# Kernel optimization log

Measured on AMD Instinct MI355X. Metric: run time of the kernel, lower is better.

Reference implementation:

```python
import jax, jax.numpy as jnp
import numpy as np

IN_F = 4096
OUT_F = 4096
RANK = 8
ALPHA = 8
SCALE = ALPHA / RANK


def setup_inputs() -> dict:
    key = jax.random.key(0)
    kx, kw, kb, ka = jax.random.split(key, 4)
    x = jax.random.normal(kx, (4, 4096, IN_F), dtype=jnp.float32)
    # base frozen linear params (torch Linear default init style, any values ok)
    W = jax.random.normal(kw, (OUT_F, IN_F), dtype=jnp.float32) * (1.0 / np.sqrt(IN_F))
    b = jax.random.normal(kb, (OUT_F,), dtype=jnp.float32) * 0.01
    # lora_A: kaiming_uniform_(a=sqrt(5)) -> U(-bound, bound), bound = sqrt(6/((1+5)*in_f)) = 1/sqrt(in_f)
    bound = 1.0 / np.sqrt(IN_F)
    lora_A = jax.random.uniform(ka, (RANK, IN_F), dtype=jnp.float32, minval=-bound, maxval=bound)
    # lora_B initialized to zeros per module; use small random values so the LoRA path is exercised
    lora_B = jax.random.normal(jax.random.fold_in(key, 7), (OUT_F, RANK), dtype=jnp.float32) * 0.02
    return {"x": x, "W": W, "b": b, "lora_A": lora_A, "lora_B": lora_B}


def reference(x, W, b, lora_A, lora_B):
    # base: x @ W.T + b  [B,S,out_f]
    base = jnp.einsum("bsi,oi->bso", x, W) + b
    # low-rank path: (x @ A.T) @ B.T * scale
    xa = jnp.einsum("bsi,ri->bsr", x, lora_A)  # [B,S,r]
    lora = jnp.einsum("bsr,or->bso", xa, lora_B)
    return base + lora * SCALE
```

## Files before the change

kernel.cpp:

```cpp
#include <hip/hip_runtime.h>
#include <cstdint>

#define K_IN   4096
#define N_OUT  4096
#define M_ROWS 16384
#define RANK   8
#define LSCALE 1.0f
#define NTILES 128

typedef __attribute__((ext_vector_type(8))) short  short8;
typedef __attribute__((ext_vector_type(4))) float  floatx4;

__device__ __forceinline__ unsigned short f2bf(float f) {
  uint32_t u = __float_as_uint(f);
  u += 0x7FFFu + ((u >> 16) & 1u);
  return (unsigned short)(u >> 16);
}

__global__ __launch_bounds__(256) void fold_w_kernel(
    const float* __restrict__ W, const float* __restrict__ lA,
    const float* __restrict__ lB, unsigned short* __restrict__ Weff) {
  int idx = blockIdx.x * 256 + threadIdx.x;
  int o = idx >> 10;
  int k = (idx & 1023) << 2;
  float4 w = *reinterpret_cast<const float4*>(W + (size_t)o * K_IN + k);
#pragma unroll
  for (int r = 0; r < RANK; ++r) {
    float s = LSCALE * lB[o * RANK + r];
    float4 a = *reinterpret_cast<const float4*>(lA + r * K_IN + k);
    w.x += s * a.x; w.y += s * a.y; w.z += s * a.z; w.w += s * a.w;
  }
  ushort4 p;
  p.x = f2bf(w.x); p.y = f2bf(w.y); p.z = f2bf(w.z); p.w = f2bf(w.w);
  *reinterpret_cast<ushort4*>(Weff + (size_t)o * K_IN + k) = p;
}

__global__ __launch_bounds__(256) void cvt_x_kernel(
    const float* __restrict__ x, unsigned short* __restrict__ xb) {
  size_t i = ((size_t)blockIdx.x * 256 + threadIdx.x) * 8;
  float4 a = *reinterpret_cast<const float4*>(x + i);
  float4 c = *reinterpret_cast<const float4*>(x + i + 4);
  uint4 v;
  v.x = (uint32_t)f2bf(a.x) | ((uint32_t)f2bf(a.y) << 16);
  v.y = (uint32_t)f2bf(a.z) | ((uint32_t)f2bf(a.w) << 16);
  v.z = (uint32_t)f2bf(c.x) | ((uint32_t)f2bf(c.y) << 16);
  v.w = (uint32_t)f2bf(c.z) | ((uint32_t)f2bf(c.w) << 16);
  *reinterpret_cast<uint4*>(xb + i) = v;
}

__device__ __forceinline__ void gload_lds16(const void* g, void* l) {
  __builtin_amdgcn_global_load_lds(
      (const __attribute__((address_space(1))) void*)g,
      (__attribute__((address_space(3))) void*)l, 16, 0, 0);
}

__global__ __launch_bounds__(512, 2) void gemm_kernel(
    const unsigned short* __restrict__ Xb, const unsigned short* __restrict__ Wb,
    const float* __restrict__ bias, float* __restrict__ out) {
  __shared__ alignas(16) char lds[4 * 32768];

  const int tid  = threadIdx.x;
  const int wave = tid >> 6, lane = tid & 63;
  const int wr = wave >> 2, wc = wave & 3;
  const int l15 = lane & 15, sq = lane >> 4;

  int bx  = blockIdx.x;
  int sbx = (bx & 7) * 128 + (bx >> 3);
  const int mt = sbx >> 4;
  const int nt = sbx & 15;

  const unsigned short *gA0, *gA1, *gB0, *gB1;
  {
    int L0 = (wave * 2 + 0) * 1024 + lane * 16;
    int r0 = ((L0 >> 7) << 1) | (((L0 >> 6) ^ (L0 >> 8)) & 1);
    int s0 = ((L0 >> 4) & 3) ^ (r0 & 3);
    gA0 = Xb + (size_t)(mt * 256 + r0) * K_IN + s0 * 8;
    gB0 = Wb + (size_t)(nt * 256 + r0) * K_IN + s0 * 8;
    int L1 = (wave * 2 + 1) * 1024 + lane * 16;
    int r1 = ((L1 >> 7) << 1) | (((L1 >> 6) ^ (L1 >> 8)) & 1);
    int s1 = ((L1 >> 4) & 3) ^ (r1 & 3);
    gA1 = Xb + (size_t)(mt * 256 + r1) * K_IN + s1 * 8;
    gB1 = Wb + (size_t)(nt * 256 + r1) * K_IN + s1 * 8;
  }
  const int lo0 = (wave * 2 + 0) * 1024;
  const int lo1 = (wave * 2 + 1) * 1024;

#define STAGE(tt) do {                                        \
    char* base_ = lds + ((tt) & 3) * 32768;                   \
    gload_lds16(gA0 + (tt) * 32, base_ + lo0);                \
    gload_lds16(gB0 + (tt) * 32, base_ + 16384 + lo0);        \
    gload_lds16(gA1 + (tt) * 32, base_ + lo1);                \
    gload_lds16(gB1 + (tt) * 32, base_ + 16384 + lo1);        \
  } while (0)

  floatx4 acc[8][4];
#pragma unroll
  for (int i = 0; i < 8; ++i)
#pragma unroll
    for (int j = 0; j < 4; ++j)
      acc[i][j] = (floatx4){0.f, 0.f, 0.f, 0.f};

  STAGE(0); STAGE(1); STAGE(2);

  const int xorv = (l15 & 7) << 4;

  for (int t = 0; t < NTILES; ++t) {
    if (t < NTILES - 2)       asm volatile("s_waitcnt vmcnt(8)" ::: "memory");
    else if (t == NTILES - 2) asm volatile("s_waitcnt vmcnt(4)" ::: "memory");
    else                      asm volatile("s_waitcnt vmcnt(0)" ::: "memory");
    __builtin_amdgcn_s_barrier();
    asm volatile("" ::: "memory");

    const char* Ab = lds + (t & 3) * 32768;
    const char* Bb = Ab + 16384;
    short8 af[8], bf[4];
#pragma unroll
    for (int i = 0; i < 8; ++i) {
      int rA = wr * 128 + i * 16 + l15;
      int LA = ((rA << 6) | (sq << 4)) ^ xorv;
      af[i] = *reinterpret_cast<const short8*>(Ab + LA);
    }
#pragma unroll
    for (int j = 0; j < 4; ++j) {
      int rB = wc * 64 + j * 16 + l15;
      int LB = ((rB << 6) | (sq << 4)) ^ xorv;
      bf[j] = *reinterpret_cast<const short8*>(Bb + LB);
    }
    asm volatile("s_waitcnt lgkmcnt(0)" ::: "memory");
    __builtin_amdgcn_s_barrier();
    asm volatile("" ::: "memory");

    if (t + 3 < NTILES) STAGE(t + 3);

#pragma unroll
    for (int i = 0; i < 8; ++i)
#pragma unroll
      for (int j = 0; j < 4; ++j)
        acc[i][j] = __builtin_amdgcn_mfma_f32_16x16x32_bf16(af[i], bf[j], acc[i][j], 0, 0, 0);
  }
#undef STAGE

  const int row0 = mt * 256 + wr * 128 + sq * 4;
  const int col0 = nt * 256 + wc * 64 + l15;
#pragma unroll
  for (int j = 0; j < 4; ++j) {
    int col = col0 + j * 16;
    float bv = bias[col];
#pragma unroll
    for (int i = 0; i < 8; ++i) {
      int rowb = row0 + i * 16;
#pragma unroll
      for (int rr = 0; rr < 4; ++rr)
        out[(size_t)(rowb + rr) * N_OUT + col] = acc[i][j][rr] + bv;
    }
  }
}

__global__ __launch_bounds__(256) void fallback_kernel(
    const float* __restrict__ x, const float* __restrict__ W,
    const float* __restrict__ bias, const float* __restrict__ lA,
    const float* __restrict__ lB, float* __restrict__ out) {
  __shared__ float Xs[64][17];
  __shared__ float Ws[64][17];
  int tid = threadIdx.x;
  int tx = tid & 15, ty = tid >> 4;
  int bm = blockIdx.y * 64, bn = blockIdx.x * 64;
  float acc[4][4] = {};
  for (int k0 = 0; k0 < K_IN; k0 += 16) {
#pragma unroll
    for (int q = 0; q < 4; ++q) {
      int flat = q * 256 + tid;
      int r = flat >> 4, c = flat & 15;
      Xs[r][c] = x[(size_t)(bm + r) * K_IN + k0 + c];
      float w = W[(size_t)(bn + r) * K_IN + k0 + c];
#pragma unroll
      for (int rr = 0; rr < RANK; ++rr)
        w += LSCALE * lB[(bn + r) * RANK + rr] * lA[rr * K_IN + k0 + c];
      Ws[r][c] = w;
    }
    __syncthreads();
#pragma unroll
    for (int kk = 0; kk < 16; ++kk) {
      float av[4], bv[4];
#pragma unroll
      for (int i = 0; i < 4; ++i) av[i] = Xs[ty * 4 + i][kk];
#pragma unroll
      for (int j = 0; j < 4; ++j) bv[j] = Ws[tx * 4 + j][kk];
#pragma unroll
      for (int i = 0; i < 4; ++i)
#pragma unroll
        for (int j = 0; j < 4; ++j) acc[i][j] += av[i] * bv[j];
    }
    __syncthreads();
  }
#pragma unroll
  for (int i = 0; i < 4; ++i)
#pragma unroll
    for (int j = 0; j < 4; ++j)
      out[(size_t)(bm + ty * 4 + i) * N_OUT + bn + tx * 4 + j] =
          acc[i][j] + bias[bn + tx * 4 + j];
}

extern "C" void kernel_launch(void* const* d_in, const int* in_sizes, int n_in,
                              void* d_out, int out_size, void* d_ws, size_t ws_size,
                              hipStream_t stream) {
  const float* x  = (const float*)d_in[0];
  const float* W  = (const float*)d_in[1];
  const float* b  = (const float*)d_in[2];
  const float* lA = (const float*)d_in[3];
  const float* lB = (const float*)d_in[4];
  float* out = (float*)d_out;

  const size_t weff_bytes = (size_t)N_OUT * K_IN * 2;
  const size_t xb_bytes   = (size_t)M_ROWS * K_IN * 2;

  if (ws_size >= weff_bytes + xb_bytes) {
    unsigned short* Weff = (unsigned short*)d_ws;
    unsigned short* Xb   = (unsigned short*)((char*)d_ws + weff_bytes);
    fold_w_kernel<<<(int)(((size_t)N_OUT * K_IN / 4) / 256), 256, 0, stream>>>(W, lA, lB, Weff);
    cvt_x_kernel<<<(int)(((size_t)M_ROWS * K_IN / 8) / 256), 256, 0, stream>>>(x, Xb);
    gemm_kernel<<<(M_ROWS / 256) * (N_OUT / 256), 512, 0, stream>>>(Xb, Weff, b, out);
  } else {
    dim3 grid(N_OUT / 64, M_ROWS / 64);
    fallback_kernel<<<grid, 256, 0, stream>>>(x, W, b, lA, lB, out);
  }
}
```

Measured before the change: 711.6 us.

## Restructure GEMM main loop into 8-phase double-buffered schedule with MFMA priority

Replaces the four-stage K=32 LDS ring with two 64 KB buffers, each holding a K=64 tile split into two K-halves. Each tile is processed in four phases that interleave LDS fragment loads, the next tile's global-to-LDS loads, and half of the MFMAs, with s_setprio raised around MFMA bursts. The aim is to overlap memory traffic with compute more finely and to cut register pressure by holding only four A fragments at a time. The cost is many more barriers per K step and shallower prefetch depth, and the hand-placed vmcnt waits must be correct for the LDS reuse to be safe.

```diff
diff --git a/kernel.cpp b/kernel.cpp
--- a/kernel.cpp
+++ b/kernel.cpp
@@ -6,7 +6,7 @@
 #define M_ROWS 16384
 #define RANK   8
 #define LSCALE 1.0f
-#define NTILES 128
+#define NT     64
 
 typedef __attribute__((ext_vector_type(8))) short  short8;
 typedef __attribute__((ext_vector_type(4))) float  floatx4;
@@ -57,12 +57,13 @@
 __global__ __launch_bounds__(512, 2) void gemm_kernel(
     const unsigned short* __restrict__ Xb, const unsigned short* __restrict__ Wb,
     const float* __restrict__ bias, float* __restrict__ out) {
-  __shared__ alignas(16) char lds[4 * 32768];
+  __shared__ alignas(16) char lds[2 * 65536];
 
   const int tid  = threadIdx.x;
   const int wave = tid >> 6, lane = tid & 63;
   const int wr = wave >> 2, wc = wave & 3;
   const int l15 = lane & 15, sq = lane >> 4;
+  const int xorv = (l15 & 7) << 4;
 
   int bx  = blockIdx.x;
   int sbx = (bx & 7) * 128 + (bx >> 3);
@@ -71,27 +72,57 @@
 
   const unsigned short *gA0, *gA1, *gB0, *gB1;
   {
-    int L0 = (wave * 2 + 0) * 1024 + lane * 16;
+    int L0 = tid * 16;
     int r0 = ((L0 >> 7) << 1) | (((L0 >> 6) ^ (L0 >> 8)) & 1);
     int s0 = ((L0 >> 4) & 3) ^ (r0 & 3);
     gA0 = Xb + (size_t)(mt * 256 + r0) * K_IN + s0 * 8;
     gB0 = Wb + (size_t)(nt * 256 + r0) * K_IN + s0 * 8;
-    int L1 = (wave * 2 + 1) * 1024 + lane * 16;
+    int L1 = 8192 + tid * 16;
     int r1 = ((L1 >> 7) << 1) | (((L1 >> 6) ^ (L1 >> 8)) & 1);
     int s1 = ((L1 >> 4) & 3) ^ (r1 & 3);
     gA1 = Xb + (size_t)(mt * 256 + r1) * K_IN + s1 * 8;
     gB1 = Wb + (size_t)(nt * 256 + r1) * K_IN + s1 * 8;
   }
-  const int lo0 = (wave * 2 + 0) * 1024;
-  const int lo1 = (wave * 2 + 1) * 1024;
-
-#define STAGE(tt) do {                                        \
-    char* base_ = lds + ((tt) & 3) * 32768;                   \
-    gload_lds16(gA0 + (tt) * 32, base_ + lo0);                \
-    gload_lds16(gB0 + (tt) * 32, base_ + 16384 + lo0);        \
-    gload_lds16(gA1 + (tt) * 32, base_ + lo1);                \
-    gload_lds16(gB1 + (tt) * 32, base_ + 16384 + lo1);        \
+
+#define STAGE_A(TT, KS) do {                                         \
+    char* d_ = lds + ((TT) & 1) * 65536 + (KS) * 16384 + tid * 16;   \
+    gload_lds16(gA0 + (TT) * 64 + (KS) * 32, d_);                    \
+    gload_lds16(gA1 + (TT) * 64 + (KS) * 32, d_ + 8192);             \
   } while (0)
+#define STAGE_B(TT, KS) do {                                         \
+    char* d_ = lds + ((TT) & 1) * 65536 + 32768 + (KS) * 16384 + tid * 16; \
+    gload_lds16(gB0 + (TT) * 64 + (KS) * 32, d_);                    \
+    gload_lds16(gB1 + (TT) * 64 + (KS) * 32, d_ + 8192);             \
+  } while (0)
+#define BAR() do { asm volatile("" ::: "memory");                    \
+    __builtin_amdgcn_s_barrier();                                    \
+    asm volatile("" ::: "memory"); } while (0)
+#define LGKM0() asm volatile("s_waitcnt lgkmcnt(0)" ::: "memory")
+#define LOAD_AF(MH, KS) do {                                         \
+    const char* Ah_ = lds + tb + (KS) * 16384;                       \
+    _Pragma("unroll")                                                \
+    for (int i = 0; i < 4; ++i) {                                    \
+      int rA_ = wr * 128 + ((MH) * 4 + i) * 16 + l15;                \
+      int LA_ = ((rA_ << 6) | (sq << 4)) ^ xorv;                     \
+      af[i] = *reinterpret_cast<const short8*>(Ah_ + LA_);           \
+    } } while (0)
+#define LOAD_BF(KS) do {                                             \
+    const char* Bh_ = lds + tb + 32768 + (KS) * 16384;               \
+    _Pragma("unroll")                                                \
+    for (int j = 0; j < 4; ++j) {                                    \
+      int rB_ = wc * 64 + j * 16 + l15;                              \
+      int LB_ = ((rB_ << 6) | (sq << 4)) ^ xorv;                     \
+      bf[j] = *reinterpret_cast<const short8*>(Bh_ + LB_);           \
+    } } while (0)
+#define DO_MFMA(MH) do {                                             \
+    __builtin_amdgcn_s_setprio(1);                                   \
+    _Pragma("unroll")                                                \
+    for (int i = 0; i < 4; ++i)                                      \
+      _Pragma("unroll")                                              \
+      for (int j = 0; j < 4; ++j)                                    \
+        acc[(MH) * 4 + i][j] = __builtin_amdgcn_mfma_f32_16x16x32_bf16( \
+            af[i], bf[j], acc[(MH) * 4 + i][j], 0, 0, 0);            \
+    __builtin_amdgcn_s_setprio(0); } while (0)
 
   floatx4 acc[8][4];
 #pragma unroll
@@ -100,45 +131,50 @@
     for (int j = 0; j < 4; ++j)
       acc[i][j] = (floatx4){0.f, 0.f, 0.f, 0.f};
 
-  STAGE(0); STAGE(1); STAGE(2);
-
-  const int xorv = (l15 & 7) << 4;
-
-  for (int t = 0; t < NTILES; ++t) {
-    if (t < NTILES - 2)       asm volatile("s_waitcnt vmcnt(8)" ::: "memory");
-    else if (t == NTILES - 2) asm volatile("s_waitcnt vmcnt(4)" ::: "memory");
-    else                      asm volatile("s_waitcnt vmcnt(0)" ::: "memory");
-    __builtin_amdgcn_s_barrier();
-    asm volatile("" ::: "memory");
-
-    const char* Ab = lds + (t & 3) * 32768;
-    const char* Bb = Ab + 16384;
-    short8 af[8], bf[4];
-#pragma unroll
-    for (int i = 0; i < 8; ++i) {
-      int rA = wr * 128 + i * 16 + l15;
-      int LA = ((rA << 6) | (sq << 4)) ^ xorv;
-      af[i] = *reinterpret_cast<const short8*>(Ab + LA);
-    }
-#pragma unroll
-    for (int j = 0; j < 4; ++j) {
-      int rB = wc * 64 + j * 16 + l15;
-      int LB = ((rB << 6) | (sq << 4)) ^ xorv;
-      bf[j] = *reinterpret_cast<const short8*>(Bb + LB);
-    }
-    asm volatile("s_waitcnt lgkmcnt(0)" ::: "memory");
-    __builtin_amdgcn_s_barrier();
-    asm volatile("" ::: "memory");
-
-    if (t + 3 < NTILES) STAGE(t + 3);
-
-#pragma unroll
-    for (int i = 0; i < 8; ++i)
-#pragma unroll
-      for (int j = 0; j < 4; ++j)
-        acc[i][j] = __builtin_amdgcn_mfma_f32_16x16x32_bf16(af[i], bf[j], acc[i][j], 0, 0, 0);
-  }
-#undef STAGE
+  STAGE_A(0, 0); STAGE_B(0, 0); STAGE_A(0, 1); STAGE_B(0, 1);
+  asm volatile("s_waitcnt vmcnt(4)" ::: "memory");
+  BAR();
+
+  short8 af[4], bf[4];
+
+  for (int t = 0; t < NT; ++t) {
+    const int tb = (t & 1) * 65536;
+    const bool more = (t + 1 < NT);
+
+    LOAD_AF(0, 0);
+    LOAD_BF(0);
+    if (more) STAGE_A(t + 1, 0);
+    BAR(); LGKM0();
+    DO_MFMA(0);
+    BAR();
+
+    LOAD_AF(1, 0);
+    if (more) STAGE_B(t + 1, 0);
+    BAR(); LGKM0();
+    DO_MFMA(1);
+    if (more) asm volatile("s_waitcnt vmcnt(4)" ::: "memory");
+    else      asm volatile("s_waitcnt vmcnt(0)" ::: "memory");
+    BAR();
+
+    LOAD_AF(0, 1);
+    LOAD_BF(1);
+    if (more) STAGE_A(t + 1, 1);
+    BAR(); LGKM0();
+    DO_MFMA(0);
+    BAR();
+
+    LOAD_AF(1, 1);
+    if (more) STAGE_B(t + 1, 1);
+    BAR(); LGKM0();
+    DO_MFMA(1);
+    if (more) asm volatile("s_waitcnt vmcnt(4)" ::: "memory");
+    BAR();
+  }
+#undef STAGE_A
+#undef STAGE_B
+#undef LOAD_AF
+#undef LOAD_BF
+#undef DO_MFMA
 
   const int row0 = mt * 256 + wr * 128 + sq * 4;
   const int col0 = nt * 256 + wc * 64 + l15;
```

Result: faster. 638.9 us (-10.2%).

## Restructure GEMM mainloop into quadrant-interleaved 8-wave ping-pong with K=64 tiles

Applied to the files above, without the earlier changes.

Reworks the bf16 GEMM main loop to use 64-wide K tiles double-buffered in LDS, staged in quarter-tile chunks interleaved between four MFMA quadrant phases separated by barriers. Adds s_setprio around MFMA bursts and a new XOR swizzle for 128-byte rows. The aim is finer-grained overlap of global->LDS loads, LDS reads and MFMA issue, plus fewer iterations. It adds more barriers per iteration and relies on careful vmcnt accounting, which risks correctness or stalls.

```diff
diff --git a/kernel.cpp b/kernel.cpp
--- a/kernel.cpp
+++ b/kernel.cpp
@@ -6,7 +6,9 @@
 #define M_ROWS 16384
 #define RANK   8
 #define LSCALE 1.0f
-#define NTILES 128
+#define NT     64
+#define ROWB   8192
+#define AHALF  1048576
 
 typedef __attribute__((ext_vector_type(8))) short  short8;
 typedef __attribute__((ext_vector_type(4))) float  floatx4;
@@ -57,7 +59,7 @@
 __global__ __launch_bounds__(512, 2) void gemm_kernel(
     const unsigned short* __restrict__ Xb, const unsigned short* __restrict__ Wb,
     const float* __restrict__ bias, float* __restrict__ out) {
-  __shared__ alignas(16) char lds[4 * 32768];
+  __shared__ alignas(16) char lds[2 * 65536];
 
   const int tid  = threadIdx.x;
   const int wave = tid >> 6, lane = tid & 63;
@@ -69,29 +71,59 @@
   const int mt = sbx >> 4;
   const int nt = sbx & 15;
 
-  const unsigned short *gA0, *gA1, *gB0, *gB1;
-  {
-    int L0 = (wave * 2 + 0) * 1024 + lane * 16;
-    int r0 = ((L0 >> 7) << 1) | (((L0 >> 6) ^ (L0 >> 8)) & 1);
-    int s0 = ((L0 >> 4) & 3) ^ (r0 & 3);
-    gA0 = Xb + (size_t)(mt * 256 + r0) * K_IN + s0 * 8;
-    gB0 = Wb + (size_t)(nt * 256 + r0) * K_IN + s0 * 8;
-    int L1 = (wave * 2 + 1) * 1024 + lane * 16;
-    int r1 = ((L1 >> 7) << 1) | (((L1 >> 6) ^ (L1 >> 8)) & 1);
-    int s1 = ((L1 >> 4) & 3) ^ (r1 & 3);
-    gA1 = Xb + (size_t)(mt * 256 + r1) * K_IN + s1 * 8;
-    gB1 = Wb + (size_t)(nt * 256 + r1) * K_IN + s1 * 8;
-  }
-  const int lo0 = (wave * 2 + 0) * 1024;
-  const int lo1 = (wave * 2 + 1) * 1024;
-
-#define STAGE(tt) do {                                        \
-    char* base_ = lds + ((tt) & 3) * 32768;                   \
-    gload_lds16(gA0 + (tt) * 32, base_ + lo0);                \
-    gload_lds16(gB0 + (tt) * 32, base_ + 16384 + lo0);        \
-    gload_lds16(gA1 + (tt) * 32, base_ + lo1);                \
-    gload_lds16(gB1 + (tt) * 32, base_ + 16384 + lo1);        \
+  const int rstg = tid >> 3;
+  const int cbst = ((tid & 7) << 4) ^ (tid & 32);
+  const char* aBase = (const char*)Xb + (size_t)(mt * 256 + rstg) * ROWB + cbst;
+  const char* bBase = (const char*)Wb + (size_t)(nt * 256 + rstg) * ROWB + cbst;
+
+#define STAGE(H) do {                                                     \
+    int th_ = (H) >> 2, hh_ = (H) & 3;                                    \
+    const char* src_ = ((hh_ < 2) ? aBase + (size_t)hh_ * AHALF           \
+                                  : bBase + (size_t)(hh_ - 2) * AHALF)    \
+                       + th_ * 128;                                       \
+    char* dst_ = lds + (th_ & 1) * 65536 + hh_ * 16384 + tid * 16;        \
+    gload_lds16(src_, dst_);                                              \
+    gload_lds16(src_ + (size_t)64 * ROWB, dst_ + 8192);                   \
   } while (0)
+#define BAR() do { asm volatile("" ::: "memory");                         \
+    __builtin_amdgcn_s_barrier();                                         \
+    asm volatile("" ::: "memory"); } while (0)
+#define LDSWZ(ROW, COLB) ((((ROW) << 7) | (COLB)) ^ (((ROW) & 4) << 3))
+#define LOAD_A(DST, MQ) do {                                              \
+    const char* Ab_ = lds + tb + wr * 16384;                              \
+    _Pragma("unroll")                                                     \
+    for (int ks = 0; ks < 2; ++ks)                                        \
+      _Pragma("unroll")                                                   \
+      for (int fi = 0; fi < 4; ++fi) {                                    \
+        int row_ = (MQ) * 64 + fi * 16 + l15;                             \
+        int cb_  = ks * 64 + sq * 16;                                     \
+        DST[ks * 4 + fi] =                                                \
+            *reinterpret_cast<const short8*>(Ab_ + LDSWZ(row_, cb_));     \
+      } } while (0)
+#define LOAD_B(DST, NQ) do {                                              \
+    const char* Bb_ = lds + tb + (2 + (wc >> 1)) * 16384;                 \
+    _Pragma("unroll")                                                     \
+    for (int ks = 0; ks < 2; ++ks)                                        \
+      _Pragma("unroll")                                                   \
+      for (int fj = 0; fj < 2; ++fj) {                                    \
+        int row_ = (wc & 1) * 64 + (NQ) * 32 + fj * 16 + l15;             \
+        int cb_  = ks * 64 + sq * 16;                                     \
+        DST[ks * 2 + fj] =                                                \
+            *reinterpret_cast<const short8*>(Bb_ + LDSWZ(row_, cb_));     \
+      } } while (0)
+#define MFMA_Q(MQ, NQ, AF, BF) do {                                       \
+    __builtin_amdgcn_s_setprio(1);                                        \
+    _Pragma("unroll")                                                     \
+    for (int ks = 0; ks < 2; ++ks)                                        \
+      _Pragma("unroll")                                                   \
+      for (int fi = 0; fi < 4; ++fi)                                      \
+        _Pragma("unroll")                                                 \
+        for (int fj = 0; fj < 2; ++fj)                                    \
+          acc[(MQ) * 4 + fi][(NQ) * 2 + fj] =                             \
+              __builtin_amdgcn_mfma_f32_16x16x32_bf16(                    \
+                  AF[ks * 4 + fi], BF[ks * 2 + fj],                       \
+                  acc[(MQ) * 4 + fi][(NQ) * 2 + fj], 0, 0, 0);            \
+    __builtin_amdgcn_s_setprio(0); } while (0)
 
   floatx4 acc[8][4];
 #pragma unroll
@@ -100,45 +132,46 @@
     for (int j = 0; j < 4; ++j)
       acc[i][j] = (floatx4){0.f, 0.f, 0.f, 0.f};
 
-  STAGE(0); STAGE(1); STAGE(2);
-
-  const int xorv = (l15 & 7) << 4;
-
-  for (int t = 0; t < NTILES; ++t) {
-    if (t < NTILES - 2)       asm volatile("s_waitcnt vmcnt(8)" ::: "memory");
-    else if (t == NTILES - 2) asm volatile("s_waitcnt vmcnt(4)" ::: "memory");
-    else                      asm volatile("s_waitcnt vmcnt(0)" ::: "memory");
-    __builtin_amdgcn_s_barrier();
-    asm volatile("" ::: "memory");
-
-    const char* Ab = lds + (t & 3) * 32768;
-    const char* Bb = Ab + 16384;
-    short8 af[8], bf[4];
-#pragma unroll
-    for (int i = 0; i < 8; ++i) {
-      int rA = wr * 128 + i * 16 + l15;
-      int LA = ((rA << 6) | (sq << 4)) ^ xorv;
-      af[i] = *reinterpret_cast<const short8*>(Ab + LA);
-    }
-#pragma unroll
-    for (int j = 0; j < 4; ++j) {
-      int rB = wc * 64 + j * 16 + l15;
-      int LB = ((rB << 6) | (sq << 4)) ^ xorv;
-      bf[j] = *reinterpret_cast<const short8*>(Bb + LB);
-    }
-    asm volatile("s_waitcnt lgkmcnt(0)" ::: "memory");
-    __builtin_amdgcn_s_barrier();
-    asm volatile("" ::: "memory");
-
-    if (t + 3 < NTILES) STAGE(t + 3);
-
-#pragma unroll
-    for (int i = 0; i < 8; ++i)
-#pragma unroll
-      for (int j = 0; j < 4; ++j)
-        acc[i][j] = __builtin_amdgcn_mfma_f32_16x16x32_bf16(af[i], bf[j], acc[i][j], 0, 0, 0);
+  for (int h = 0; h < 7; ++h) STAGE(h);
+  asm volatile("s_waitcnt vmcnt(6)" ::: "memory");
+  BAR();
+
+  short8 afA[8], afB[8], bfC[4];
+
+  for (int t = 0; t < NT; ++t) {
+    const int tb = (t & 1) * 65536;
+    const int p0 = 4 * t;
+
+    LOAD_A(afA, 0);
+    LOAD_B(bfC, 0);
+    if (p0 + 7 < 4 * NT) STAGE(p0 + 7);
+    BAR();
+    MFMA_Q(0, 0, afA, bfC);
+    BAR();
+
+    LOAD_A(afB, 1);
+    if (p0 + 8 < 4 * NT) STAGE(p0 + 8);
+    BAR();
+    MFMA_Q(1, 0, afB, bfC);
+    BAR();
+
+    LOAD_B(bfC, 1);
+    if (p0 + 9 < 4 * NT) STAGE(p0 + 9);
+    BAR();
+    MFMA_Q(1, 1, afB, bfC);
+    BAR();
+
+    if (p0 + 10 < 4 * NT) STAGE(p0 + 10);
+    if (t <= NT - 3)      asm volatile("s_waitcnt vmcnt(6)" ::: "memory");
+    else if (t == NT - 2) asm volatile("s_waitcnt vmcnt(0)" ::: "memory");
+    BAR();
+    MFMA_Q(0, 1, afA, bfC);
+    BAR();
   }
 #undef STAGE
+#undef LOAD_A
+#undef LOAD_B
+#undef MFMA_Q
 
   const int row0 = mt * 256 + wr * 128 + sq * 4;
   const int col0 = nt * 256 + wc * 64 + l15;
```

New measurement: 630.3 us. -11.4%, faster.
